# Kernel tuning notes

Hardware: AMD Instinct MI355X
Metric: run time of the kernel (lower is better)

## Reference

```python
import jax, jax.numpy as jnp
import numpy as np

N_HEADS = 16
HIDDEN = 1024
HEAD = HIDDEN // N_HEADS


def setup_inputs() -> dict:
    key = jax.random.key(0)
    ks = jax.random.split(key, 11)
    B, S, H = 2, 2048, HIDDEN
    s = 1.0 / np.sqrt(H)
    return {
        "query": jax.random.normal(ks[0], (B, S, H), jnp.float32),
        "key": jax.random.normal(ks[1], (B, S, H), jnp.float32),
        "value": jax.random.normal(ks[2], (B, S, H), jnp.float32),
        "Wq": jax.random.normal(ks[3], (H, H), jnp.float32) * s,
        "bq": jnp.zeros((H,), jnp.float32),
        "Wk": jax.random.normal(ks[4], (H, H), jnp.float32) * s,
        "bk": jnp.zeros((H,), jnp.float32),
        "Wv": jax.random.normal(ks[5], (H, H), jnp.float32) * s,
        "bv": jnp.zeros((H,), jnp.float32),
        "Wo": jax.random.normal(ks[6], (H, H), jnp.float32) * s,
        "bo": jnp.zeros((H,), jnp.float32),
    }


def reference(query, key, value, Wq, bq, Wk, bk, Wv, bv, Wo, bo):
    B, Sq, H = query.shape
    Sk = key.shape[1]
    # QKV projections, split heads: [B, n_heads, S, head]
    q = (query @ Wq + bq).reshape(B, Sq, N_HEADS, HEAD).transpose(0, 2, 1, 3)
    k = (key @ Wk + bk).reshape(B, Sk, N_HEADS, HEAD).transpose(0, 2, 1, 3)
    v = (value @ Wv + bv).reshape(B, Sk, N_HEADS, HEAD).transpose(0, 2, 1, 3)
    # scaled dot-product attention (no mask, dropout p=0)
    scores = jnp.einsum("bhqd,bhkd->bhqk", q, k) / np.sqrt(HEAD).astype(np.float32)
    attn = jax.nn.softmax(scores, axis=-1)
    out = jnp.einsum("bhqk,bhkd->bhqd", attn, v)
    out = out.transpose(0, 2, 1, 3).reshape(B, Sq, H)
    return out @ Wo + bo
```

## Files before the change

### kernel.cpp

```cpp
#include <hip/hip_runtime.h>
#include <hip/hip_bf16.h>
#include <stdint.h>

typedef unsigned short u16;
typedef short bf16x8 __attribute__((ext_vector_type(8)));
typedef float f32x4 __attribute__((ext_vector_type(4)));

#define DEVI static __device__ __forceinline__

#if __has_builtin(__builtin_amdgcn_exp2f)
#define EXP2F(x) __builtin_amdgcn_exp2f(x)
#else
#define EXP2F(x) exp2f(x)
#endif

DEVI u16 f2bf(float f) {
  union { float f; uint32_t u; } v; v.f = f;
  uint32_t u = v.u;
  u += 0x7fffu + ((u >> 16) & 1u);
  return (u16)(u >> 16);
}
DEVI uint32_t pk2bf(float lo, float hi) {
  __hip_bfloat162 h = __float22bfloat162_rn(float2{lo, hi});
  union { __hip_bfloat162 h; uint32_t u; } v; v.h = h; return v.u;
}

DEVI void async16(const void* g, const void* l) {
  __builtin_amdgcn_global_load_lds(
      (const __attribute__((address_space(1))) void*)g,
      (__attribute__((address_space(3))) void*)l, 16, 0, 0);
}

DEVI f32x4 mfma16(bf16x8 a, bf16x8 b, f32x4 c) {
  return __builtin_amdgcn_mfma_f32_16x16x32_bf16(a, b, c, 0, 0, 0);
}

#define CSC 0.18033688011112042f

__global__ void convx(const float* __restrict__ q, const float* __restrict__ k,
                      const float* __restrict__ v, u16* __restrict__ out) {
  const int z = blockIdx.y;
  const float* src = (z == 0) ? q : (z == 1) ? k : v;
  const int i = (blockIdx.x * 256 + threadIdx.x) * 4;
  float4 f = *(const float4*)(src + i);
  ushort4 o;
  o.x = f2bf(f.x); o.y = f2bf(f.y); o.z = f2bf(f.z); o.w = f2bf(f.w);
  *(ushort4*)(out + (size_t)z * 4194304 + i) = o;
}

__global__ void transw(const float* __restrict__ Wq, const float* __restrict__ Wk,
                       const float* __restrict__ Wv, const float* __restrict__ Wo,
                       u16* __restrict__ WT) {
  __shared__ u16 tile[64 * 68];
  const int z = blockIdx.z;
  const float* W = (z == 0) ? Wq : (z == 1) ? Wk : (z == 2) ? Wv : Wo;
  u16* out = WT + (size_t)z * 1048576;
  const int R0 = blockIdx.y * 64, C0 = blockIdx.x * 64;
  const int t = threadIdx.x;
#pragma unroll
  for (int it = 0; it < 16; ++it) {
    int j = it * 256 + t;
    int r = j >> 6, c = j & 63;
    tile[r * 68 + c] = f2bf(W[(size_t)(R0 + r) * 1024 + C0 + c]);
  }
  __syncthreads();
#pragma unroll
  for (int it = 0; it < 16; ++it) {
    int j = it * 256 + t;
    int c = j >> 6, r = j & 63;
    out[(size_t)(C0 + c) * 1024 + R0 + r] = tile[r * 68 + c];
  }
}

__global__ __launch_bounds__(256, 3)
void qkv_gemm(const u16* __restrict__ XB, const u16* __restrict__ WT,
              const float* __restrict__ bq, const float* __restrict__ bk,
              const float* __restrict__ bv,
              u16* __restrict__ QN, u16* __restrict__ KN, u16* __restrict__ VT) {
  __shared__ u16 smem[16896];
  u16* lA = smem;
  u16* lB = smem + 8192;
  const int z = blockIdx.y;
  const u16* A  = XB + (size_t)z * 4194304;
  const u16* Bt = WT + (size_t)z * 1048576;
  const float* bias = (z == 0) ? bq : (z == 1) ? bk : bv;
  const int T = blockIdx.x;
  const int m0 = (T & 31) * 128, n0 = (T >> 5) * 128;
  const int t = threadIdx.x, lane = t & 63, w = t >> 6;
  const int quad = lane >> 4, l16 = lane & 15;
  const int wm = (w & 1) * 64, wn = (w >> 1) * 64;

  f32x4 acc[4][4] = {};
  for (int kt = 0; kt < 16; ++kt) {
    const int k0 = kt * 64;
#pragma unroll
    for (int it = 0; it < 4; ++it) {
      int i = it * 256 + t;
      int r = i >> 3, cc = i & 7, c = cc ^ (r & 7);
      async16(A + (size_t)(m0 + r) * 1024 + k0 + c * 8, &lA[i * 8]);
      async16(Bt + (size_t)(n0 + r) * 1024 + k0 + c * 8, &lB[i * 8]);
    }
    __syncthreads();
#pragma unroll
    for (int ks = 0; ks < 2; ++ks) {
      bf16x8 af[4], bfr[4];
#pragma unroll
      for (int rt = 0; rt < 4; ++rt) {
        int row = wm + rt * 16 + l16;
        af[rt] = *(const bf16x8*)&lA[row * 64 + ((ks * 4 + quad) ^ (row & 7)) * 8];
      }
#pragma unroll
      for (int ct = 0; ct < 4; ++ct) {
        int row = wn + ct * 16 + l16;
        bfr[ct] = *(const bf16x8*)&lB[row * 64 + ((ks * 4 + quad) ^ (row & 7)) * 8];
      }
#pragma unroll
      for (int rt = 0; rt < 4; ++rt)
#pragma unroll
        for (int ct = 0; ct < 4; ++ct)
          acc[rt][ct] = mfma16(bfr[ct], af[rt], acc[rt][ct]);
    }
    __syncthreads();
  }

  if (z < 2) {
    const float scl = (z == 0) ? CSC : 1.0f;
#pragma unroll
    for (int rt = 0; rt < 4; ++rt) {
      int sl = wm + rt * 16 + l16;
#pragma unroll
      for (int ct = 0; ct < 4; ++ct) {
        int nb = wn + ct * 16 + quad * 4;
        float4 b4 = *(const float4*)&bias[n0 + nb];
        ushort4 pk;
        pk.x = f2bf((acc[rt][ct][0] + b4.x) * scl);
        pk.y = f2bf((acc[rt][ct][1] + b4.y) * scl);
        pk.z = f2bf((acc[rt][ct][2] + b4.z) * scl);
        pk.w = f2bf((acc[rt][ct][3] + b4.w) * scl);
        *(ushort4*)&smem[sl * 132 + nb] = pk;
      }
    }
    __syncthreads();
    u16* out = (z == 0) ? QN : KN;
#pragma unroll
    for (int p = 0; p < 8; ++p) {
      int idx = p * 256 + t;
      int row = idx >> 4, chunk = idx & 15;
      *(bf16x8*)&out[(size_t)(m0 + row) * 1024 + n0 + chunk * 8] =
          *(const bf16x8*)&smem[row * 132 + chunk * 8];
    }
  } else {
#pragma unroll
    for (int rt = 0; rt < 4; ++rt) {
      int sl = wm + rt * 16 + l16;
#pragma unroll
      for (int ct = 0; ct < 4; ++ct) {
        int nb = wn + ct * 16 + quad * 4;
        float4 b4 = *(const float4*)&bias[n0 + nb];
        smem[(nb + 0) * 132 + sl] = f2bf(acc[rt][ct][0] + b4.x);
        smem[(nb + 1) * 132 + sl] = f2bf(acc[rt][ct][1] + b4.y);
        smem[(nb + 2) * 132 + sl] = f2bf(acc[rt][ct][2] + b4.z);
        smem[(nb + 3) * 132 + sl] = f2bf(acc[rt][ct][3] + b4.w);
      }
    }
    __syncthreads();
    const int bb = m0 >> 11, sb = m0 & 2047;
#pragma unroll
    for (int p = 0; p < 8; ++p) {
      int idx = p * 256 + t;
      int dl = idx >> 4, chunk = idx & 15;
      int ncol = n0 + dl, hh = ncol >> 6, dd = ncol & 63;
      *(bf16x8*)&VT[((size_t)((bb * 16 + hh) * 64 + dd)) * 2048 + sb + chunk * 8] =
          *(const bf16x8*)&smem[dl * 132 + chunk * 8];
    }
  }
}

__global__ __launch_bounds__(512, 4)
void attn5(const u16* __restrict__ QN, const u16* __restrict__ KN,
           const u16* __restrict__ VT, u16* __restrict__ AO) {
  __shared__ u16 lK[2][64 * 64];
  __shared__ u16 lV[2][64 * 64];
  __shared__ u16 lPT[8][16 * 72];
  const int qt0 = blockIdx.x, h = blockIdx.y, b = blockIdx.z;
  const int t = threadIdx.x, lane = t & 63, w = t >> 6;
  const int quad = lane >> 4, l16 = lane & 15;
  const u16* Qg = QN + ((size_t)(b * 2048 + qt0 * 128)) * 1024 + h * 64;
  const u16* Kg = KN + ((size_t)b * 2048) * 1024 + h * 64;
  const u16* Vg = VT + ((size_t)((b * 16 + h) * 64)) * 2048;

  bf16x8 qf[2];
#pragma unroll
  for (int ks = 0; ks < 2; ++ks)
    qf[ks] = *(const bf16x8*)(Qg + (size_t)(w * 16 + l16) * 1024 + ks * 32 + quad * 8);

  {
    int r = t >> 3, cc = t & 7, c = cc ^ (r & 7);
    async16(Kg + (size_t)r * 1024 + c * 8, &lK[0][t * 8]);
    async16(Vg + (size_t)r * 2048 + c * 8, &lV[0][t * 8]);
  }
  __syncthreads();

  f32x4 o[4] = {};
  float lsum = 0.f;
  u16* myP = &lPT[w][0];

  for (int kt = 0; kt < 32; ++kt) {
    const int cur = kt & 1, nxt = cur ^ 1;
    if (kt + 1 < 32) {
      const int kb = (kt + 1) * 64;
      int r = t >> 3, cc = t & 7, c = cc ^ (r & 7);
      async16(Kg + (size_t)(kb + r) * 1024 + c * 8, &lK[nxt][t * 8]);
      async16(Vg + (size_t)r * 2048 + kb + c * 8, &lV[nxt][t * 8]);
    }

    f32x4 sc[4];
#pragma unroll
    for (int st = 0; st < 4; ++st) {
      int row = st * 16 + l16;
      bf16x8 kf0 = *(const bf16x8*)&lK[cur][row * 64 + ((quad) ^ (row & 7)) * 8];
      bf16x8 kf1 = *(const bf16x8*)&lK[cur][row * 64 + ((4 + quad) ^ (row & 7)) * 8];
      f32x4 z = {};
      sc[st] = mfma16(kf0, qf[0], z);
      sc[st] = mfma16(kf1, qf[1], sc[st]);
    }

#pragma unroll
    for (int st = 0; st < 4; ++st) {
      float p0 = EXP2F(sc[st][0]);
      float p1 = EXP2F(sc[st][1]);
      float p2 = EXP2F(sc[st][2]);
      float p3 = EXP2F(sc[st][3]);
      lsum += (p0 + p1) + (p2 + p3);
      uint2 pk;
      pk.x = pk2bf(p0, p1);
      pk.y = pk2bf(p2, p3);
      *(uint2*)&myP[l16 * 72 + st * 16 + quad * 4] = pk;
    }

#pragma unroll
    for (int ks2 = 0; ks2 < 2; ++ks2) {
      bf16x8 pf = *(const bf16x8*)&myP[l16 * 72 + ks2 * 32 + quad * 8];
#pragma unroll
      for (int dt = 0; dt < 4; ++dt) {
        int row = dt * 16 + l16;
        bf16x8 vf = *(const bf16x8*)&lV[cur][row * 64 + ((ks2 * 4 + quad) ^ (row & 7)) * 8];
        o[dt] = mfma16(vf, pf, o[dt]);
      }
    }
    __syncthreads();
  }

  float l = lsum;
  l += __shfl_xor(l, 16, 64);
  l += __shfl_xor(l, 32, 64);
  float inv = 1.0f / l;
  int qglob = qt0 * 128 + w * 16 + l16;
  size_t base = ((size_t)(b * 2048 + qglob)) * 1024 + h * 64;
#pragma unroll
  for (int dt = 0; dt < 4; ++dt) {
    ushort4 pk;
    pk.x = f2bf(o[dt][0] * inv);
    pk.y = f2bf(o[dt][1] * inv);
    pk.z = f2bf(o[dt][2] * inv);
    pk.w = f2bf(o[dt][3] * inv);
    *(ushort4*)&AO[base + dt * 16 + quad * 4] = pk;
  }
}

__global__ __launch_bounds__(256, 2)
void oproj_gemm(const u16* __restrict__ AO, const u16* __restrict__ Bt,
                const float* __restrict__ bias, float* __restrict__ out) {
  __shared__ u16 lA[128 * 64];
  __shared__ u16 lB[64 * 64];
  const int T = blockIdx.x;
  const int m0 = (T & 31) * 128, n0 = (T >> 5) * 64;
  const int t = threadIdx.x, lane = t & 63, w = t >> 6;
  const int quad = lane >> 4, l16 = lane & 15;
  const int wm = (w & 1) * 64, wn = (w >> 1) * 32;

  f32x4 acc[4][2] = {};
  for (int kt = 0; kt < 16; ++kt) {
    const int k0 = kt * 64;
#pragma unroll
    for (int it = 0; it < 4; ++it) {
      int i = it * 256 + t;
      int r = i >> 3, cc = i & 7, c = cc ^ (r & 7);
      async16(AO + (size_t)(m0 + r) * 1024 + k0 + c * 8, &lA[i * 8]);
    }
#pragma unroll
    for (int it = 0; it < 2; ++it) {
      int i = it * 256 + t;
      int r = i >> 3, cc = i & 7, c = cc ^ (r & 7);
      async16(Bt + (size_t)(n0 + r) * 1024 + k0 + c * 8, &lB[i * 8]);
    }
    __syncthreads();
#pragma unroll
    for (int ks = 0; ks < 2; ++ks) {
      bf16x8 af[4], bfr[2];
#pragma unroll
      for (int rt = 0; rt < 4; ++rt) {
        int row = wm + rt * 16 + l16;
        af[rt] = *(const bf16x8*)&lA[row * 64 + ((ks * 4 + quad) ^ (row & 7)) * 8];
      }
#pragma unroll
      for (int ct = 0; ct < 2; ++ct) {
        int row = wn + ct * 16 + l16;
        bfr[ct] = *(const bf16x8*)&lB[row * 64 + ((ks * 4 + quad) ^ (row & 7)) * 8];
      }
#pragma unroll
      for (int rt = 0; rt < 4; ++rt)
#pragma unroll
        for (int ct = 0; ct < 2; ++ct)
          acc[rt][ct] = mfma16(af[rt], bfr[ct], acc[rt][ct]);
    }
    __syncthreads();
  }

#pragma unroll
  for (int ct = 0; ct < 2; ++ct) {
    int ncol = n0 + wn + ct * 16 + l16;
    float bvv = bias[ncol];
#pragma unroll
    for (int rt = 0; rt < 4; ++rt)
#pragma unroll
      for (int r = 0; r < 4; ++r) {
        int m = m0 + wm + rt * 16 + quad * 4 + r;
        out[(size_t)m * 1024 + ncol] = acc[rt][ct][r] + bvv;
      }
  }
}

extern "C" void kernel_launch(void* const* d_in, const int* in_sizes, int n_in,
                              void* d_out, int out_size, void* d_ws, size_t ws_size,
                              hipStream_t stream) {
  const float* query = (const float*)d_in[0];
  const float* key   = (const float*)d_in[1];
  const float* value = (const float*)d_in[2];
  const float* Wq = (const float*)d_in[3];
  const float* bq = (const float*)d_in[4];
  const float* Wk = (const float*)d_in[5];
  const float* bk = (const float*)d_in[6];
  const float* Wv = (const float*)d_in[7];
  const float* bv = (const float*)d_in[8];
  const float* Wo = (const float*)d_in[9];
  const float* bo = (const float*)d_in[10];
  float* out = (float*)d_out;

  u16* WT = (u16*)d_ws;
  u16* QN = WT + 4 * 1048576;
  u16* KN = QN + 4194304;
  u16* VT = KN + 4194304;
  u16* XB = VT + 4194304;
  u16* AO = XB;

  convx<<<dim3(4096, 3), 256, 0, stream>>>(query, key, value, XB);
  transw<<<dim3(16, 16, 4), 256, 0, stream>>>(Wq, Wk, Wv, Wo, WT);
  qkv_gemm<<<dim3(256, 3), 256, 0, stream>>>(XB, WT, bq, bk, bv, QN, KN, VT);
  attn5<<<dim3(16, 16, 2), 512, 0, stream>>>(QN, KN, VT, AO);
  oproj_gemm<<<dim3(512), 256, 0, stream>>>(AO, WT + 3 * 1048576, bo, out);
}
```

Before: 218.7 us.

## Use 32x32 MFMA in attention with split-KV wave pairs and LDS reduction

The attention kernel moves from 16x16x32 to 32x32x16 bf16 MFMA tiles. Each pair of waves shares a 32-query group and splits every 64-key tile into two 32-key halves, cutting LDS fragment reloads per MFMA. Partial outputs and row sums from the second wave of each pair go through LDS in bf16 and are merged at the end. This adds an epilogue reduction and one extra sync, and rounds the partial sums to bf16 before the merge.

```diff
diff --git a/kernel.cpp b/kernel.cpp
--- a/kernel.cpp
+++ b/kernel.cpp
@@ -5,6 +5,7 @@
 typedef unsigned short u16;
 typedef short bf16x8 __attribute__((ext_vector_type(8)));
 typedef float f32x4 __attribute__((ext_vector_type(4)));
+typedef float f32x16 __attribute__((ext_vector_type(16)));
 
 #define DEVI static __device__ __forceinline__
 
@@ -24,6 +25,9 @@
   __hip_bfloat162 h = __float22bfloat162_rn(float2{lo, hi});
   union { __hip_bfloat162 h; uint32_t u; } v; v.h = h; return v.u;
 }
+DEVI float bf2f(u16 u) {
+  union { uint32_t u; float f; } v; v.u = ((uint32_t)u) << 16; return v.f;
+}
 
 DEVI void async16(const void* g, const void* l) {
   __builtin_amdgcn_global_load_lds(
@@ -33,6 +37,9 @@
 
 DEVI f32x4 mfma16(bf16x8 a, bf16x8 b, f32x4 c) {
   return __builtin_amdgcn_mfma_f32_16x16x32_bf16(a, b, c, 0, 0, 0);
+}
+DEVI f32x16 mfma32(bf16x8 a, bf16x8 b, f32x16 c) {
+  return __builtin_amdgcn_mfma_f32_32x32x16_bf16(a, b, c, 0, 0, 0);
 }
 
 #define CSC 0.18033688011112042f
@@ -177,94 +184,119 @@
 }
 
 __global__ __launch_bounds__(512, 4)
-void attn5(const u16* __restrict__ QN, const u16* __restrict__ KN,
+void attn6(const u16* __restrict__ QN, const u16* __restrict__ KN,
            const u16* __restrict__ VT, u16* __restrict__ AO) {
-  __shared__ u16 lK[2][64 * 64];
-  __shared__ u16 lV[2][64 * 64];
-  __shared__ u16 lPT[8][16 * 72];
+  __shared__ u16 lK[2][4096];
+  __shared__ u16 lV[2][4096];
+  __shared__ u16 lP[8][1152];
   const int qt0 = blockIdx.x, h = blockIdx.y, b = blockIdx.z;
   const int t = threadIdx.x, lane = t & 63, w = t >> 6;
-  const int quad = lane >> 4, l16 = lane & 15;
+  const int l32 = lane & 31, hf = lane >> 5;
+  const int qg = w >> 1, sg = w & 1;
   const u16* Qg = QN + ((size_t)(b * 2048 + qt0 * 128)) * 1024 + h * 64;
   const u16* Kg = KN + ((size_t)b * 2048) * 1024 + h * 64;
   const u16* Vg = VT + ((size_t)((b * 16 + h) * 64)) * 2048;
 
-  bf16x8 qf[2];
-#pragma unroll
-  for (int ks = 0; ks < 2; ++ks)
-    qf[ks] = *(const bf16x8*)(Qg + (size_t)(w * 16 + l16) * 1024 + ks * 32 + quad * 8);
+  bf16x8 qf[4];
+#pragma unroll
+  for (int ks = 0; ks < 4; ++ks)
+    qf[ks] = *(const bf16x8*)(Qg + (size_t)(qg * 32 + l32) * 1024 + ks * 16 + hf * 8);
 
   {
-    int r = t >> 3, cc = t & 7, c = cc ^ (r & 7);
-    async16(Kg + (size_t)r * 1024 + c * 8, &lK[0][t * 8]);
-    async16(Vg + (size_t)r * 2048 + c * 8, &lV[0][t * 8]);
+    int r = t >> 3, cl = (t & 7) ^ (r & 7);
+    async16(Kg + (size_t)r * 1024 + cl * 8, &lK[0][t * 8]);
+    async16(Vg + (size_t)r * 2048 + cl * 8, &lV[0][t * 8]);
   }
   __syncthreads();
 
-  f32x4 o[4] = {};
+  f32x16 o[2] = {};
   float lsum = 0.f;
-  u16* myP = &lPT[w][0];
+  u16* myP = &lP[w][0];
 
   for (int kt = 0; kt < 32; ++kt) {
     const int cur = kt & 1, nxt = cur ^ 1;
     if (kt + 1 < 32) {
       const int kb = (kt + 1) * 64;
-      int r = t >> 3, cc = t & 7, c = cc ^ (r & 7);
-      async16(Kg + (size_t)(kb + r) * 1024 + c * 8, &lK[nxt][t * 8]);
-      async16(Vg + (size_t)r * 2048 + kb + c * 8, &lV[nxt][t * 8]);
-    }
-
-    f32x4 sc[4];
-#pragma unroll
-    for (int st = 0; st < 4; ++st) {
-      int row = st * 16 + l16;
-      bf16x8 kf0 = *(const bf16x8*)&lK[cur][row * 64 + ((quad) ^ (row & 7)) * 8];
-      bf16x8 kf1 = *(const bf16x8*)&lK[cur][row * 64 + ((4 + quad) ^ (row & 7)) * 8];
-      f32x4 z = {};
-      sc[st] = mfma16(kf0, qf[0], z);
-      sc[st] = mfma16(kf1, qf[1], sc[st]);
-    }
-
-#pragma unroll
-    for (int st = 0; st < 4; ++st) {
-      float p0 = EXP2F(sc[st][0]);
-      float p1 = EXP2F(sc[st][1]);
-      float p2 = EXP2F(sc[st][2]);
-      float p3 = EXP2F(sc[st][3]);
+      int r = t >> 3, cl = (t & 7) ^ (r & 7);
+      async16(Kg + (size_t)(kb + r) * 1024 + cl * 8, &lK[nxt][t * 8]);
+      async16(Vg + (size_t)r * 2048 + kb + cl * 8, &lV[nxt][t * 8]);
+    }
+
+    f32x16 sc;
+    {
+      int r = sg * 32 + l32;
+#pragma unroll
+      for (int ks = 0; ks < 4; ++ks) {
+        int c = (ks * 2 + hf) ^ (r & 7);
+        bf16x8 kf = *(const bf16x8*)&lK[cur][r * 64 + c * 8];
+        if (ks == 0) { f32x16 z = {}; sc = mfma32(kf, qf[0], z); }
+        else sc = mfma32(kf, qf[ks], sc);
+      }
+    }
+
+#pragma unroll
+    for (int g = 0; g < 4; ++g) {
+      float p0 = EXP2F(sc[4 * g + 0]);
+      float p1 = EXP2F(sc[4 * g + 1]);
+      float p2 = EXP2F(sc[4 * g + 2]);
+      float p3 = EXP2F(sc[4 * g + 3]);
       lsum += (p0 + p1) + (p2 + p3);
       uint2 pk;
       pk.x = pk2bf(p0, p1);
       pk.y = pk2bf(p2, p3);
-      *(uint2*)&myP[l16 * 72 + st * 16 + quad * 4] = pk;
+      *(uint2*)&myP[l32 * 36 + g * 8 + hf * 4] = pk;
     }
 
 #pragma unroll
     for (int ks2 = 0; ks2 < 2; ++ks2) {
-      bf16x8 pf = *(const bf16x8*)&myP[l16 * 72 + ks2 * 32 + quad * 8];
-#pragma unroll
-      for (int dt = 0; dt < 4; ++dt) {
-        int row = dt * 16 + l16;
-        bf16x8 vf = *(const bf16x8*)&lV[cur][row * 64 + ((ks2 * 4 + quad) ^ (row & 7)) * 8];
-        o[dt] = mfma16(vf, pf, o[dt]);
-      }
-    }
-    __syncthreads();
-  }
-
-  float l = lsum;
-  l += __shfl_xor(l, 16, 64);
-  l += __shfl_xor(l, 32, 64);
-  float inv = 1.0f / l;
-  int qglob = qt0 * 128 + w * 16 + l16;
-  size_t base = ((size_t)(b * 2048 + qglob)) * 1024 + h * 64;
-#pragma unroll
-  for (int dt = 0; dt < 4; ++dt) {
-    ushort4 pk;
-    pk.x = f2bf(o[dt][0] * inv);
-    pk.y = f2bf(o[dt][1] * inv);
-    pk.z = f2bf(o[dt][2] * inv);
-    pk.w = f2bf(o[dt][3] * inv);
-    *(ushort4*)&AO[base + dt * 16 + quad * 4] = pk;
+      bf16x8 pf = *(const bf16x8*)&myP[l32 * 36 + ks2 * 16 + hf * 8];
+#pragma unroll
+      for (int dt = 0; dt < 2; ++dt) {
+        int r = dt * 32 + l32;
+        int c = (sg * 4 + ks2 * 2 + hf) ^ (r & 7);
+        bf16x8 vf = *(const bf16x8*)&lV[cur][r * 64 + c * 8];
+        o[dt] = mfma32(vf, pf, o[dt]);
+      }
+    }
+    __syncthreads();
+  }
+
+  lsum += __shfl_xor(lsum, 32, 64);
+  u16* cbuf = &lP[0][0];
+  float* lbufF = (float*)&lK[0][0];
+  if (sg == 1) {
+    if (lane < 32) lbufF[qg * 32 + lane] = lsum;
+#pragma unroll
+    for (int dt = 0; dt < 2; ++dt)
+#pragma unroll
+      for (int g = 0; g < 4; ++g) {
+        int d = dt * 32 + 8 * g + 4 * hf;
+        ushort4 pk;
+        pk.x = f2bf(o[dt][4 * g + 0]);
+        pk.y = f2bf(o[dt][4 * g + 1]);
+        pk.z = f2bf(o[dt][4 * g + 2]);
+        pk.w = f2bf(o[dt][4 * g + 3]);
+        *(ushort4*)&cbuf[(qg * 32 + l32) * 68 + d] = pk;
+      }
+  }
+  __syncthreads();
+  if (sg == 0) {
+    float inv = 1.0f / (lsum + lbufF[qg * 32 + l32]);
+    int q = qt0 * 128 + qg * 32 + l32;
+    size_t base = ((size_t)(b * 2048 + q)) * 1024 + h * 64;
+#pragma unroll
+    for (int dt = 0; dt < 2; ++dt)
+#pragma unroll
+      for (int g = 0; g < 4; ++g) {
+        int d = dt * 32 + 8 * g + 4 * hf;
+        ushort4 pp = *(const ushort4*)&cbuf[(qg * 32 + l32) * 68 + d];
+        ushort4 pk;
+        pk.x = f2bf((o[dt][4 * g + 0] + bf2f(pp.x)) * inv);
+        pk.y = f2bf((o[dt][4 * g + 1] + bf2f(pp.y)) * inv);
+        pk.z = f2bf((o[dt][4 * g + 2] + bf2f(pp.z)) * inv);
+        pk.w = f2bf((o[dt][4 * g + 3] + bf2f(pp.w)) * inv);
+        *(ushort4*)&AO[base + d] = pk;
+      }
   }
 }
 
@@ -357,6 +389,6 @@
   convx<<<dim3(4096, 3), 256, 0, stream>>>(query, key, value, XB);
   transw<<<dim3(16, 16, 4), 256, 0, stream>>>(Wq, Wk, Wv, Wo, WT);
   qkv_gemm<<<dim3(256, 3), 256, 0, stream>>>(XB, WT, bq, bk, bv, QN, KN, VT);
-  attn5<<<dim3(16, 16, 2), 512, 0, stream>>>(QN, KN, VT, AO);
+  attn6<<<dim3(16, 16, 2), 512, 0, stream>>>(QN, KN, VT, AO);
   oproj_gemm<<<dim3(512), 256, 0, stream>>>(AO, WT + 3 * 1048576, bo, out);
 }
```

Result: slower. 233.2 us (+6.6%).

## Give each attention wave two query subtiles to reuse K/V fragments

Applied to the files above, without the earlier changes.

The attention kernel drops from 8 waves per block to 4. Each wave now processes 32 query rows as two 16-row subtiles, so every K and V fragment read from shared memory feeds two MFMAs instead of one. This halves LDS fragment traffic per FLOP, but doubles per-wave register use and lowers waves per block. The grid is also reordered with heads on blockIdx.x, which changes the order in which blocks touch K/V and may affect cache locality. Softmax still uses the pre-scaled exp2 with no running max, as before.

```diff
diff --git a/kernel.cpp b/kernel.cpp
--- a/kernel.cpp
+++ b/kernel.cpp
@@ -176,95 +176,115 @@
   }
 }
 
-__global__ __launch_bounds__(512, 4)
-void attn5(const u16* __restrict__ QN, const u16* __restrict__ KN,
+__global__ __launch_bounds__(256, 3)
+void attn7(const u16* __restrict__ QN, const u16* __restrict__ KN,
            const u16* __restrict__ VT, u16* __restrict__ AO) {
   __shared__ u16 lK[2][64 * 64];
   __shared__ u16 lV[2][64 * 64];
-  __shared__ u16 lPT[8][16 * 72];
-  const int qt0 = blockIdx.x, h = blockIdx.y, b = blockIdx.z;
+  __shared__ u16 lPT[4][32 * 72];
+  const int h = blockIdx.x, qt0 = blockIdx.y, b = blockIdx.z;
   const int t = threadIdx.x, lane = t & 63, w = t >> 6;
   const int quad = lane >> 4, l16 = lane & 15;
   const u16* Qg = QN + ((size_t)(b * 2048 + qt0 * 128)) * 1024 + h * 64;
   const u16* Kg = KN + ((size_t)b * 2048) * 1024 + h * 64;
   const u16* Vg = VT + ((size_t)((b * 16 + h) * 64)) * 2048;
 
-  bf16x8 qf[2];
-#pragma unroll
-  for (int ks = 0; ks < 2; ++ks)
-    qf[ks] = *(const bf16x8*)(Qg + (size_t)(w * 16 + l16) * 1024 + ks * 32 + quad * 8);
-
-  {
-    int r = t >> 3, cc = t & 7, c = cc ^ (r & 7);
-    async16(Kg + (size_t)r * 1024 + c * 8, &lK[0][t * 8]);
-    async16(Vg + (size_t)r * 2048 + c * 8, &lV[0][t * 8]);
+  bf16x8 qf[2][2];
+#pragma unroll
+  for (int qt = 0; qt < 2; ++qt)
+#pragma unroll
+    for (int ks = 0; ks < 2; ++ks)
+      qf[qt][ks] = *(const bf16x8*)(Qg + (size_t)(w * 32 + qt * 16 + l16) * 1024 +
+                                    ks * 32 + quad * 8);
+
+#pragma unroll
+  for (int it = 0; it < 2; ++it) {
+    int s = it * 256 + t;
+    int r = s >> 3, cc = s & 7, c = cc ^ (r & 7);
+    async16(Kg + (size_t)r * 1024 + c * 8, &lK[0][s * 8]);
+    async16(Vg + (size_t)r * 2048 + c * 8, &lV[0][s * 8]);
   }
   __syncthreads();
 
-  f32x4 o[4] = {};
-  float lsum = 0.f;
+  f32x4 o[2][4] = {};
+  float lsum[2] = {0.f, 0.f};
   u16* myP = &lPT[w][0];
 
   for (int kt = 0; kt < 32; ++kt) {
     const int cur = kt & 1, nxt = cur ^ 1;
     if (kt + 1 < 32) {
       const int kb = (kt + 1) * 64;
-      int r = t >> 3, cc = t & 7, c = cc ^ (r & 7);
-      async16(Kg + (size_t)(kb + r) * 1024 + c * 8, &lK[nxt][t * 8]);
-      async16(Vg + (size_t)r * 2048 + kb + c * 8, &lV[nxt][t * 8]);
-    }
-
-    f32x4 sc[4];
+#pragma unroll
+      for (int it = 0; it < 2; ++it) {
+        int s = it * 256 + t;
+        int r = s >> 3, cc = s & 7, c = cc ^ (r & 7);
+        async16(Kg + (size_t)(kb + r) * 1024 + c * 8, &lK[nxt][s * 8]);
+        async16(Vg + (size_t)r * 2048 + kb + c * 8, &lV[nxt][s * 8]);
+      }
+    }
+
+    f32x4 sc[2][4];
 #pragma unroll
     for (int st = 0; st < 4; ++st) {
       int row = st * 16 + l16;
       bf16x8 kf0 = *(const bf16x8*)&lK[cur][row * 64 + ((quad) ^ (row & 7)) * 8];
       bf16x8 kf1 = *(const bf16x8*)&lK[cur][row * 64 + ((4 + quad) ^ (row & 7)) * 8];
       f32x4 z = {};
-      sc[st] = mfma16(kf0, qf[0], z);
-      sc[st] = mfma16(kf1, qf[1], sc[st]);
-    }
-
-#pragma unroll
-    for (int st = 0; st < 4; ++st) {
-      float p0 = EXP2F(sc[st][0]);
-      float p1 = EXP2F(sc[st][1]);
-      float p2 = EXP2F(sc[st][2]);
-      float p3 = EXP2F(sc[st][3]);
-      lsum += (p0 + p1) + (p2 + p3);
-      uint2 pk;
-      pk.x = pk2bf(p0, p1);
-      pk.y = pk2bf(p2, p3);
-      *(uint2*)&myP[l16 * 72 + st * 16 + quad * 4] = pk;
+      sc[0][st] = mfma16(kf0, qf[0][0], z);
+      sc[0][st] = mfma16(kf1, qf[0][1], sc[0][st]);
+      sc[1][st] = mfma16(kf0, qf[1][0], z);
+      sc[1][st] = mfma16(kf1, qf[1][1], sc[1][st]);
+    }
+
+#pragma unroll
+    for (int qt = 0; qt < 2; ++qt) {
+      int prow = qt * 16 + l16;
+#pragma unroll
+      for (int st = 0; st < 4; ++st) {
+        float p0 = EXP2F(sc[qt][st][0]);
+        float p1 = EXP2F(sc[qt][st][1]);
+        float p2 = EXP2F(sc[qt][st][2]);
+        float p3 = EXP2F(sc[qt][st][3]);
+        lsum[qt] += (p0 + p1) + (p2 + p3);
+        uint2 pk;
+        pk.x = pk2bf(p0, p1);
+        pk.y = pk2bf(p2, p3);
+        *(uint2*)&myP[prow * 72 + st * 16 + quad * 4] = pk;
+      }
     }
 
 #pragma unroll
     for (int ks2 = 0; ks2 < 2; ++ks2) {
-      bf16x8 pf = *(const bf16x8*)&myP[l16 * 72 + ks2 * 32 + quad * 8];
+      bf16x8 pf0 = *(const bf16x8*)&myP[(l16) * 72 + ks2 * 32 + quad * 8];
+      bf16x8 pf1 = *(const bf16x8*)&myP[(16 + l16) * 72 + ks2 * 32 + quad * 8];
 #pragma unroll
       for (int dt = 0; dt < 4; ++dt) {
         int row = dt * 16 + l16;
         bf16x8 vf = *(const bf16x8*)&lV[cur][row * 64 + ((ks2 * 4 + quad) ^ (row & 7)) * 8];
-        o[dt] = mfma16(vf, pf, o[dt]);
-      }
-    }
-    __syncthreads();
-  }
-
-  float l = lsum;
-  l += __shfl_xor(l, 16, 64);
-  l += __shfl_xor(l, 32, 64);
-  float inv = 1.0f / l;
-  int qglob = qt0 * 128 + w * 16 + l16;
-  size_t base = ((size_t)(b * 2048 + qglob)) * 1024 + h * 64;
-#pragma unroll
-  for (int dt = 0; dt < 4; ++dt) {
-    ushort4 pk;
-    pk.x = f2bf(o[dt][0] * inv);
-    pk.y = f2bf(o[dt][1] * inv);
-    pk.z = f2bf(o[dt][2] * inv);
-    pk.w = f2bf(o[dt][3] * inv);
-    *(ushort4*)&AO[base + dt * 16 + quad * 4] = pk;
+        o[0][dt] = mfma16(vf, pf0, o[0][dt]);
+        o[1][dt] = mfma16(vf, pf1, o[1][dt]);
+      }
+    }
+    __syncthreads();
+  }
+
+#pragma unroll
+  for (int qt = 0; qt < 2; ++qt) {
+    float l = lsum[qt];
+    l += __shfl_xor(l, 16, 64);
+    l += __shfl_xor(l, 32, 64);
+    float inv = 1.0f / l;
+    int qglob = qt0 * 128 + w * 32 + qt * 16 + l16;
+    size_t base = ((size_t)(b * 2048 + qglob)) * 1024 + h * 64;
+#pragma unroll
+    for (int dt = 0; dt < 4; ++dt) {
+      ushort4 pk;
+      pk.x = f2bf(o[qt][dt][0] * inv);
+      pk.y = f2bf(o[qt][dt][1] * inv);
+      pk.z = f2bf(o[qt][dt][2] * inv);
+      pk.w = f2bf(o[qt][dt][3] * inv);
+      *(ushort4*)&AO[base + dt * 16 + quad * 4] = pk;
+    }
   }
 }
 
@@ -357,6 +377,6 @@
   convx<<<dim3(4096, 3), 256, 0, stream>>>(query, key, value, XB);
   transw<<<dim3(16, 16, 4), 256, 0, stream>>>(Wq, Wk, Wv, Wo, WT);
   qkv_gemm<<<dim3(256, 3), 256, 0, stream>>>(XB, WT, bq, bk, bv, QN, KN, VT);
-  attn5<<<dim3(16, 16, 2), 512, 0, stream>>>(QN, KN, VT, AO);
+  attn7<<<dim3(16, 16, 2), 256, 0, stream>>>(QN, KN, VT, AO);
   oproj_gemm<<<dim3(512), 256, 0, stream>>>(AO, WT + 3 * 1048576, bo, out);
 }
```

Result: slower. 228.7 us (+4.6%).
